# Kernel tuning notes

Hardware: AMD Instinct MI355X
Metric: run time of the kernel (lower is better)

Reference implementation:

```python
import jax, jax.numpy as jnp
import numpy as np

B, N, DIM = 2, 2048, 1024
HEADS, DIM_HEAD = 16, 64
INNER = HEADS * DIM_HEAD  # 1024
SCALE = DIM_HEAD ** -0.5


def setup_inputs() -> dict:
    key = jax.random.key(0)
    ks = jax.random.split(key, 6)
    s = lambda k, shape, fan: jax.random.normal(k, shape, jnp.float32) * (fan ** -0.5)
    return {
        "x": jax.random.normal(ks[0], (B, N, DIM), jnp.float32),
        "similarity": jax.random.normal(ks[1], (B, N), jnp.float32),
        "Wq": s(ks[2], (DIM, INNER), DIM),
        "Wkv": s(ks[3], (DIM, 2 * INNER), DIM),
        "Wo": s(ks[4], (INNER, DIM), INNER),
        "bo": jnp.zeros((DIM,), jnp.float32),
    }


def reference(x, similarity, Wq, Wkv, Wo, bo):
    b, n, _ = x.shape
    h, d = HEADS, DIM_HEAD
    # projections (context = x, self-attention)
    q = (x @ Wq).reshape(b, n, h, d).transpose(0, 2, 1, 3)        # b h n d
    kv = x @ Wkv                                                   # b n 2*inner
    k, v = jnp.split(kv, 2, axis=-1)
    k = k.reshape(b, n, h, d).transpose(0, 2, 1, 3)
    v = v.reshape(b, n, h, d).transpose(0, 2, 1, 3)
    dots = jnp.einsum('bhid,bhjd->bhij', q, k) * SCALE             # b h n n
    # similarity [b,n] -> broadcast as per-query row bias [b,1,n,1]
    dots = dots + similarity[:, None, :, None]
    attn = jax.nn.softmax(dots, axis=-1)
    out = jnp.einsum('bhij,bhjd->bhid', attn, v)                   # b h n d
    out = out.transpose(0, 2, 1, 3).reshape(b, n, h * d)           # b n inner
    return out @ Wo + bo
```

## Files before the change

### kernel.cpp

```cpp
#include <hip/hip_runtime.h>


typedef __attribute__((ext_vector_type(8))) short short8;
typedef __attribute__((ext_vector_type(4))) float float4_;
typedef __attribute__((ext_vector_type(16))) float floatx16;
typedef __attribute__((ext_vector_type(4))) unsigned short ushort4_;
typedef __attribute__((ext_vector_type(4))) unsigned int uint4_;

#define MFMA(a, b, c) __builtin_amdgcn_mfma_f32_16x16x32_bf16((a), (b), (c), 0, 0, 0)
#define MFMA32(a, b, c) __builtin_amdgcn_mfma_f32_32x32x16_bf16((a), (b), (c), 0, 0, 0)

static __device__ __forceinline__ unsigned short f2bf(float f) {
    union { float f; unsigned int u; } v; v.f = f;
    unsigned int r = v.u + 0x7FFFu + ((v.u >> 16) & 1u);
    return (unsigned short)(r >> 16);
}

static __device__ __forceinline__ void gld16(const void* g, void* l) {
    __builtin_amdgcn_global_load_lds(
        (__attribute__((address_space(1))) void*)(g),
        (__attribute__((address_space(3))) void*)(l), 16, 0, 0);
}

__global__ __launch_bounds__(256) void prep(
    const float* __restrict__ X, const float* __restrict__ Wq,
    const float* __restrict__ Wkv, const float* __restrict__ Wo,
    unsigned short* __restrict__ xb, unsigned short* __restrict__ Wt,
    unsigned short* __restrict__ Wot)
{
    const int bid = blockIdx.x, t = threadIdx.x;
    if (bid >= 1024) {
        const int b = bid - 1024;
        const float4_* src = (const float4_*)X;
        ushort4_* dst = (ushort4_*)xb;
        #pragma unroll
        for (int g = 0; g < 8; ++g) {
            const int idx = b * 2048 + g * 256 + t;
            float4_ v = src[idx];
            ushort4_ o;
            o[0] = f2bf(v[0]); o[1] = f2bf(v[1]);
            o[2] = f2bf(v[2]); o[3] = f2bf(v[3]);
            dst[idx] = o;
        }
        return;
    }
    __shared__ float tile[64][65];
    const float* src; unsigned short* dst; int N, kt, nt, drow0;
    if (bid < 256)      { src = Wq;  N = 1024; kt = bid & 15;       nt = bid >> 4;       dst = Wt;  drow0 = nt * 64; }
    else if (bid < 768) { src = Wkv; N = 2048; kt = (bid-256) & 15; nt = (bid-256) >> 4; dst = Wt;  drow0 = 1024 + nt * 64; }
    else                { src = Wo;  N = 1024; kt = (bid-768) & 15; nt = (bid-768) >> 4; dst = Wot; drow0 = nt * 64; }
    const int k0 = kt * 64, n0 = nt * 64;
    const int r0 = t >> 6, c = t & 63;
    #pragma unroll
    for (int i = 0; i < 16; ++i) {
        const int r = i * 4 + r0;
        tile[r][c] = src[(size_t)(k0 + r) * N + n0 + c];
    }
    __syncthreads();
    #pragma unroll
    for (int i = 0; i < 16; ++i) {
        const int rn = i * 4 + r0;
        dst[(size_t)(drow0 + rn) * 1024 + k0 + c] = f2bf(tile[c][rn]);
    }
}

__global__ __launch_bounds__(256) void qkv_gemm2(
    const unsigned short* __restrict__ xb, const unsigned short* __restrict__ Wt,
    unsigned short* __restrict__ q_ws, unsigned short* __restrict__ k_ws,
    unsigned short* __restrict__ vt_ws)
{
    __shared__ unsigned short As[128 * 64];
    __shared__ unsigned short Bs[128 * 64];
    const int t = threadIdx.x, wave = t >> 6, lane = t & 63;
    const int L = lane & 15, quad = lane >> 4;
    const int xcd = blockIdx.x & 7, idx = blockIdx.x >> 3;
    const int mb = (xcd >> 1) * 8 + (idx & 7);
    const int nb = (xcd & 1) * 12 + (idx >> 3);
    const int m0 = mb * 128, n0 = nb * 128;
    const int wr = wave >> 1, wc = wave & 1;

    float4_ z = {0.f, 0.f, 0.f, 0.f};
    float4_ acc[4][4];
    #pragma unroll
    for (int i = 0; i < 4; ++i)
        #pragma unroll
        for (int j = 0; j < 4; ++j) acc[i][j] = z;

    const unsigned short* gA[4]; const unsigned short* gB[4];
    unsigned short* lA[4]; unsigned short* lB[4];
    #pragma unroll
    for (int j = 0; j < 4; ++j) {
        const int cid = wave * 256 + j * 64 + lane;
        const int row = cid >> 3, pc = cid & 7;
        const int lch = pc ^ (row & 7);
        gA[j] = xb + (size_t)(m0 + row) * 1024 + lch * 8;
        gB[j] = Wt + (size_t)(n0 + row) * 1024 + lch * 8;
        lA[j] = As + wave * 2048 + j * 512;
        lB[j] = Bs + wave * 2048 + j * 512;
    }

    for (int kc = 0; kc < 1024; kc += 64) {
        #pragma unroll
        for (int j = 0; j < 4; ++j) {
            gld16(gA[j] + kc, lA[j]);
            gld16(gB[j] + kc, lB[j]);
        }
        __syncthreads();
        #pragma unroll
        for (int ks = 0; ks < 2; ++ks) {
            short8 af[4], bfr[4];
            #pragma unroll
            for (int mt = 0; mt < 4; ++mt) {
                const int rl = wr * 64 + mt * 16 + L;
                af[mt] = *(const short8*)(As + rl * 64 + (((ks * 4 + quad) ^ (L & 7)) << 3));
            }
            #pragma unroll
            for (int nt = 0; nt < 4; ++nt) {
                const int rl = wc * 64 + nt * 16 + L;
                bfr[nt] = *(const short8*)(Bs + rl * 64 + (((ks * 4 + quad) ^ (L & 7)) << 3));
            }
            #pragma unroll
            for (int mt = 0; mt < 4; ++mt)
                #pragma unroll
                for (int nt = 0; nt < 4; ++nt)
                    acc[mt][nt] = MFMA(af[mt], bfr[nt], acc[mt][nt]);
        }
        __syncthreads();
    }

    const int b = m0 >> 11;
    const int type = n0 >> 10;
    #pragma unroll
    for (int mt = 0; mt < 4; ++mt) {
        const int m = (m0 & 2047) + wr * 64 + mt * 16 + quad * 4;
        #pragma unroll
        for (int nt = 0; nt < 4; ++nt) {
            const int cl = (n0 & 1023) + wc * 64 + nt * 16 + L;
            const int h = cl >> 6, d = cl & 63;
            float4_ v = acc[mt][nt];
            if (type == 0) {
                unsigned short* p = q_ws + ((size_t)(b * 16 + h) * 2048 + m) * 64 + d;
                #pragma unroll
                for (int r = 0; r < 4; ++r) p[(size_t)r * 64] = f2bf(v[r] * 0.18033688011f);
            } else if (type == 1) {
                unsigned short* p = k_ws + (size_t)(b * 16 + h) * 131072
                    + (m >> 5) * 2048 + (d >> 3) * 256 + (m & 31) * 8 + (d & 7);
                #pragma unroll
                for (int r = 0; r < 4; ++r) p[r * 8] = f2bf(v[r]);
            } else {
                ushort4_ pk;
                pk[0] = f2bf(v[0]); pk[1] = f2bf(v[1]);
                pk[2] = f2bf(v[2]); pk[3] = f2bf(v[3]);
                *(ushort4_*)(vt_ws + (size_t)(b * 16 + h) * 131072
                    + (m >> 3) * 512 + d * 8 + (m & 7)) = pk;
            }
        }
    }
}

#define LOADT(k0_, k1_, k2_, k3_, v00_, v10_, v01_, v11_, IT) do {            \
    const unsigned short* kp_ = kbase + (IT) * 2048;                          \
    const unsigned short* vp_ = vbase + (IT) * 2048;                          \
    k0_ = *(const short8*)(kp_);        k1_ = *(const short8*)(kp_ + 512);    \
    k2_ = *(const short8*)(kp_ + 1024); k3_ = *(const short8*)(kp_ + 1536);   \
    v00_ = *(const short8*)(vp_);        v10_ = *(const short8*)(vp_ + 1024); \
    v01_ = *(const short8*)(vp_ + 256);  v11_ = *(const short8*)(vp_ + 1280); \
} while (0)

#define COMPT(k0_, k1_, k2_, k3_, v00_, v10_, v01_, v11_) do {                \
    _Pragma("unroll")                                                         \
    for (int qt = 0; qt < 4; ++qt) {                                          \
        floatx16 s;                                                           \
        _Pragma("unroll")                                                     \
        for (int r = 0; r < 16; ++r) s[r] = 0.f;                              \
        s = MFMA32(k0_, qf[qt][0], s);                                        \
        s = MFMA32(k1_, qf[qt][1], s);                                        \
        s = MFMA32(k2_, qf[qt][2], s);                                        \
        s = MFMA32(k3_, qf[qt][3], s);                                        \
        unsigned int pk[8];                                                   \
        _Pragma("unroll")                                                     \
        for (int d = 0; d < 8; ++d) {                                         \
            union { float f; unsigned int u; } a_, b_;                        \
            a_.f = __builtin_amdgcn_exp2f(s[2 * d]);                          \
            b_.f = __builtin_amdgcn_exp2f(s[2 * d + 1]);                      \
            pk[d] = __builtin_amdgcn_perm(b_.u, a_.u, 0x07060302u);           \
        }                                                                     \
        uint4_ w0_, w1_;                                                      \
        w0_[0] = pk[0]; w0_[1] = pk[1]; w0_[2] = pk[2]; w0_[3] = pk[3];       \
        w1_[0] = pk[4]; w1_[1] = pk[5]; w1_[2] = pk[6]; w1_[3] = pk[7];       \
        short8 pa0 = *(short8*)&w0_, pa1 = *(short8*)&w1_;                    \
        lac[qt] = MFMA32(pa0, ONES, lac[qt]);                                 \
        lac[qt] = MFMA32(pa1, ONES, lac[qt]);                                 \
        o[qt][0] = MFMA32(pa0, v00_, o[qt][0]);                               \
        o[qt][0] = MFMA32(pa1, v10_, o[qt][0]);                               \
        o[qt][1] = MFMA32(pa0, v01_, o[qt][1]);                               \
        o[qt][1] = MFMA32(pa1, v11_, o[qt][1]);                               \
    }                                                                         \
} while (0)

__global__ __launch_bounds__(128, 1) void attn_fwd6(
    const unsigned short* __restrict__ q_ws,
    const unsigned short* __restrict__ k_ws,
    const unsigned short* __restrict__ vt_ws,
    unsigned short* __restrict__ o2)
{
    __shared__ float cb[2][6144];
    const int t = threadIdx.x, wave = t >> 6, lane = t & 63;
    const int l32 = lane & 31, hi = lane >> 5;
    const int xcd = blockIdx.x & 7, loc = blockIdx.x >> 3;
    const int bh = xcd * 4 + (loc >> 4);
    const int qb = loc & 15;

    short8 qf[4][4];
    #pragma unroll
    for (int qt = 0; qt < 4; ++qt) {
        const unsigned short* Qp = q_ws
            + ((size_t)(bh * 2048 + qb * 128 + qt * 32 + l32)) * 64 + hi * 8;
        #pragma unroll
        for (int ks = 0; ks < 4; ++ks)
            qf[qt][ks] = *(const short8*)(Qp + ks * 16);
    }

    const int piRow = (l32 & ~12) | ((l32 & 4) << 1) | ((l32 & 8) >> 1);
    const unsigned short* kbase = k_ws + (size_t)bh * 131072
        + wave * 65536 + hi * 256 + piRow * 8;
    const unsigned short* vbase = vt_ws + (size_t)bh * 131072
        + wave * 65536 + hi * 512 + l32 * 8;

    short8 ONES;
    #pragma unroll
    for (int i = 0; i < 8; ++i) ONES[i] = (short)0x3F80;

    floatx16 o[4][2], lac[4];
    #pragma unroll
    for (int qt = 0; qt < 4; ++qt) {
        #pragma unroll
        for (int r = 0; r < 16; ++r) {
            o[qt][0][r] = 0.f; o[qt][1][r] = 0.f; lac[qt][r] = 0.f;
        }
    }

    short8 kA0, kA1, kA2, kA3, vA00, vA10, vA01, vA11;
    short8 kB0, kB1, kB2, kB3, vB00, vB10, vB01, vB11;
    LOADT(kA0, kA1, kA2, kA3, vA00, vA10, vA01, vA11, 0);

    #pragma unroll 1
    for (int it = 0; it < 32; it += 2) {
        LOADT(kB0, kB1, kB2, kB3, vB00, vB10, vB01, vB11, it + 1);
        COMPT(kA0, kA1, kA2, kA3, vA00, vA10, vA01, vA11);
        LOADT(kA0, kA1, kA2, kA3, vA00, vA10, vA01, vA11, (it + 2) & 31);
        COMPT(kB0, kB1, kB2, kB3, vB00, vB10, vB01, vB11);
    }

    float* myb = cb[wave];
    const int don = wave ? 0 : 2;
    #pragma unroll
    for (int g = 0; g < 2; ++g) {
        const int qt = don + g;
        #pragma unroll
        for (int r = 0; r < 16; ++r) {
            myb[(g * 48 + r)      * 64 + lane] = o[qt][0][r];
            myb[(g * 48 + 16 + r) * 64 + lane] = o[qt][1][r];
            myb[(g * 48 + 32 + r) * 64 + lane] = lac[qt][r];
        }
    }
    __syncthreads();
    const float* otb = cb[wave ^ 1];
    const int own = wave ? 2 : 0;
    const int b = bh >> 4, h = bh & 15;
    unsigned short* obase = o2 + ((size_t)(b * 2048 + qb * 128)) * 1024 + h * 64;
    #pragma unroll
    for (int g = 0; g < 2; ++g) {
        const int qt = own + g;
        #pragma unroll
        for (int r = 0; r < 16; ++r) {
            const float o0v = o[qt][0][r] + otb[(g * 48 + r)      * 64 + lane];
            const float o1v = o[qt][1][r] + otb[(g * 48 + 16 + r) * 64 + lane];
            const float lv  = lac[qt][r]  + otb[(g * 48 + 32 + r) * 64 + lane];
            const float iv = 1.0f / lv;
            const int row = qt * 32 + (r & 3) + 8 * (r >> 2) + 4 * hi;
            obase[(size_t)row * 1024 + l32]      = f2bf(o0v * iv);
            obase[(size_t)row * 1024 + 32 + l32] = f2bf(o1v * iv);
        }
    }
}

__global__ __launch_bounds__(256) void out_gemm2(
    const unsigned short* __restrict__ o2, const unsigned short* __restrict__ Wot,
    const float* __restrict__ bo, float* __restrict__ Out)
{
    __shared__ unsigned short As[128 * 64];
    __shared__ unsigned short Bs[64 * 64];
    const int t = threadIdx.x, wave = t >> 6, lane = t & 63;
    const int L = lane & 15, quad = lane >> 4;
    const int xcd = blockIdx.x & 7, idx = blockIdx.x >> 3;
    const int mb = (xcd >> 1) * 8 + (idx & 7);
    const int nb = (xcd & 1) * 8 + (idx >> 3);
    const int m0 = mb * 128, n0 = nb * 64;
    const int wr = wave >> 1, wc = wave & 1;

    float4_ z = {0.f, 0.f, 0.f, 0.f};
    float4_ acc[4][2];
    #pragma unroll
    for (int i = 0; i < 4; ++i)
        #pragma unroll
        for (int j = 0; j < 2; ++j) acc[i][j] = z;

    const unsigned short* gA[4]; unsigned short* lA[4];
    #pragma unroll
    for (int j = 0; j < 4; ++j) {
        const int cid = wave * 256 + j * 64 + lane;
        const int row = cid >> 3, pc = cid & 7;
        gA[j] = o2 + (size_t)(m0 + row) * 1024 + (pc ^ (row & 7)) * 8;
        lA[j] = As + wave * 2048 + j * 512;
    }
    const unsigned short* gB[2]; unsigned short* lB[2];
    #pragma unroll
    for (int j = 0; j < 2; ++j) {
        const int cid = wave * 128 + j * 64 + lane;
        const int row = cid >> 3, pc = cid & 7;
        gB[j] = Wot + (size_t)(n0 + row) * 1024 + (pc ^ (row & 7)) * 8;
        lB[j] = Bs + wave * 1024 + j * 512;
    }

    for (int kc = 0; kc < 1024; kc += 64) {
        #pragma unroll
        for (int j = 0; j < 4; ++j) gld16(gA[j] + kc, lA[j]);
        #pragma unroll
        for (int j = 0; j < 2; ++j) gld16(gB[j] + kc, lB[j]);
        __syncthreads();
        #pragma unroll
        for (int ks = 0; ks < 2; ++ks) {
            short8 af[4], bfr[2];
            #pragma unroll
            for (int mt = 0; mt < 4; ++mt) {
                const int rl = wr * 64 + mt * 16 + L;
                af[mt] = *(const short8*)(As + rl * 64 + (((ks * 4 + quad) ^ (L & 7)) << 3));
            }
            #pragma unroll
            for (int nt = 0; nt < 2; ++nt) {
                const int rl = wc * 32 + nt * 16 + L;
                bfr[nt] = *(const short8*)(Bs + rl * 64 + (((ks * 4 + quad) ^ (L & 7)) << 3));
            }
            #pragma unroll
            for (int mt = 0; mt < 4; ++mt)
                #pragma unroll
                for (int nt = 0; nt < 2; ++nt)
                    acc[mt][nt] = MFMA(af[mt], bfr[nt], acc[mt][nt]);
        }
        __syncthreads();
    }

    #pragma unroll
    for (int mt = 0; mt < 4; ++mt) {
        const int m = m0 + wr * 64 + mt * 16 + quad * 4;
        #pragma unroll
        for (int nt = 0; nt < 2; ++nt) {
            const int c = n0 + wc * 32 + nt * 16 + L;
            const float bias = bo[c];
            #pragma unroll
            for (int r = 0; r < 4; ++r)
                Out[(size_t)(m + r) * 1024 + c] = acc[mt][nt][r] + bias;
        }
    }
}

extern "C" void kernel_launch(void* const* d_in, const int* in_sizes, int n_in,
                              void* d_out, int out_size, void* d_ws, size_t ws_size,
                              hipStream_t stream) {
    const float* x   = (const float*)d_in[0];
    const float* Wq  = (const float*)d_in[2];
    const float* Wkv = (const float*)d_in[3];
    const float* Wo  = (const float*)d_in[4];
    const float* bo  = (const float*)d_in[5];
    float* out = (float*)d_out;

    char* ws = (char*)d_ws;
    const size_t MB = 1024 * 1024;
    unsigned short* xb   = (unsigned short*)(ws);
    unsigned short* o2   = xb;
    unsigned short* Wt   = (unsigned short*)(ws + 8 * MB);
    unsigned short* Wot  = (unsigned short*)(ws + 14 * MB);
    unsigned short* q_ws = (unsigned short*)(ws + 16 * MB);
    unsigned short* k_ws = (unsigned short*)(ws + 24 * MB);
    unsigned short* vt_ws= (unsigned short*)(ws + 32 * MB);

    prep<<<dim3(1536), dim3(256), 0, stream>>>(x, Wq, Wkv, Wo, xb, Wt, Wot);
    qkv_gemm2<<<dim3(768), dim3(256), 0, stream>>>(xb, Wt, q_ws, k_ws, vt_ws);
    attn_fwd6<<<dim3(512), dim3(128), 0, stream>>>(q_ws, k_ws, vt_ws, o2);
    out_gemm2<<<dim3(512), dim3(256), 0, stream>>>(o2, Wot, bo, out);
}
```

Baseline: 203.2 us.

## Halve attention query tile, double grid, and compute softmax row sums on VALU

The attention kernel now handles 64 query rows per block instead of 128, launches 1024 blocks, and declares launch bounds allowing two blocks per CU, which lowers register pressure and raises occupancy. The row-sum accumulation that used extra MFMAs against a ones vector is replaced by scalar VALU adds of the exponentials, combined across lane halves with a shuffle and across waves through shared memory. This removes a third of the matrix ops in the inner loop and shrinks the shared-memory reduction buffer. In exchange, each K/V tile is reused by half as many queries, which doubles K/V load traffic per query.

```diff
diff --git a/kernel.cpp b/kernel.cpp
--- a/kernel.cpp
+++ b/kernel.cpp
@@ -169,7 +169,7 @@
 
 #define COMPT(k0_, k1_, k2_, k3_, v00_, v10_, v01_, v11_) do {                \
     _Pragma("unroll")                                                         \
-    for (int qt = 0; qt < 4; ++qt) {                                          \
+    for (int qt = 0; qt < 2; ++qt) {                                          \
         floatx16 s;                                                           \
         _Pragma("unroll")                                                     \
         for (int r = 0; r < 16; ++r) s[r] = 0.f;                              \
@@ -178,19 +178,20 @@
         s = MFMA32(k2_, qf[qt][2], s);                                        \
         s = MFMA32(k3_, qf[qt][3], s);                                        \
         unsigned int pk[8];                                                   \
+        float ls_ = 0.f;                                                      \
         _Pragma("unroll")                                                     \
         for (int d = 0; d < 8; ++d) {                                         \
             union { float f; unsigned int u; } a_, b_;                        \
             a_.f = __builtin_amdgcn_exp2f(s[2 * d]);                          \
             b_.f = __builtin_amdgcn_exp2f(s[2 * d + 1]);                      \
+            ls_ += a_.f + b_.f;                                               \
             pk[d] = __builtin_amdgcn_perm(b_.u, a_.u, 0x07060302u);           \
         }                                                                     \
+        lsum[qt] += ls_;                                                      \
         uint4_ w0_, w1_;                                                      \
         w0_[0] = pk[0]; w0_[1] = pk[1]; w0_[2] = pk[2]; w0_[3] = pk[3];       \
         w1_[0] = pk[4]; w1_[1] = pk[5]; w1_[2] = pk[6]; w1_[3] = pk[7];       \
         short8 pa0 = *(short8*)&w0_, pa1 = *(short8*)&w1_;                    \
-        lac[qt] = MFMA32(pa0, ONES, lac[qt]);                                 \
-        lac[qt] = MFMA32(pa1, ONES, lac[qt]);                                 \
         o[qt][0] = MFMA32(pa0, v00_, o[qt][0]);                               \
         o[qt][0] = MFMA32(pa1, v10_, o[qt][0]);                               \
         o[qt][1] = MFMA32(pa0, v01_, o[qt][1]);                               \
@@ -198,24 +199,25 @@
     }                                                                         \
 } while (0)
 
-__global__ __launch_bounds__(128, 1) void attn_fwd6(
+__global__ __launch_bounds__(128, 2) void attn_fwd7(
     const unsigned short* __restrict__ q_ws,
     const unsigned short* __restrict__ k_ws,
     const unsigned short* __restrict__ vt_ws,
     unsigned short* __restrict__ o2)
 {
-    __shared__ float cb[2][6144];
+    __shared__ float cbuf[2][2048];
+    __shared__ float lsd[2][2][32];
     const int t = threadIdx.x, wave = t >> 6, lane = t & 63;
     const int l32 = lane & 31, hi = lane >> 5;
     const int xcd = blockIdx.x & 7, loc = blockIdx.x >> 3;
-    const int bh = xcd * 4 + (loc >> 4);
-    const int qb = loc & 15;
-
-    short8 qf[4][4];
-    #pragma unroll
-    for (int qt = 0; qt < 4; ++qt) {
+    const int bh = xcd * 4 + (loc >> 5);
+    const int qb = loc & 31;
+
+    short8 qf[2][4];
+    #pragma unroll
+    for (int qt = 0; qt < 2; ++qt) {
         const unsigned short* Qp = q_ws
-            + ((size_t)(bh * 2048 + qb * 128 + qt * 32 + l32)) * 64 + hi * 8;
+            + ((size_t)(bh * 2048 + qb * 64 + qt * 32 + l32)) * 64 + hi * 8;
         #pragma unroll
         for (int ks = 0; ks < 4; ++ks)
             qf[qt][ks] = *(const short8*)(Qp + ks * 16);
@@ -227,18 +229,12 @@
     const unsigned short* vbase = vt_ws + (size_t)bh * 131072
         + wave * 65536 + hi * 512 + l32 * 8;
 
-    short8 ONES;
-    #pragma unroll
-    for (int i = 0; i < 8; ++i) ONES[i] = (short)0x3F80;
-
-    floatx16 o[4][2], lac[4];
-    #pragma unroll
-    for (int qt = 0; qt < 4; ++qt) {
-        #pragma unroll
-        for (int r = 0; r < 16; ++r) {
-            o[qt][0][r] = 0.f; o[qt][1][r] = 0.f; lac[qt][r] = 0.f;
-        }
-    }
+    floatx16 o[2][2];
+    float lsum[2] = {0.f, 0.f};
+    #pragma unroll
+    for (int qt = 0; qt < 2; ++qt)
+        #pragma unroll
+        for (int r = 0; r < 16; ++r) { o[qt][0][r] = 0.f; o[qt][1][r] = 0.f; }
 
     short8 kA0, kA1, kA2, kA3, vA00, vA10, vA01, vA11;
     short8 kB0, kB1, kB2, kB3, vB00, vB10, vB01, vB11;
@@ -252,36 +248,33 @@
         COMPT(kB0, kB1, kB2, kB3, vB00, vB10, vB01, vB11);
     }
 
-    float* myb = cb[wave];
-    const int don = wave ? 0 : 2;
-    #pragma unroll
-    for (int g = 0; g < 2; ++g) {
-        const int qt = don + g;
-        #pragma unroll
-        for (int r = 0; r < 16; ++r) {
-            myb[(g * 48 + r)      * 64 + lane] = o[qt][0][r];
-            myb[(g * 48 + 16 + r) * 64 + lane] = o[qt][1][r];
-            myb[(g * 48 + 32 + r) * 64 + lane] = lac[qt][r];
-        }
+    #pragma unroll
+    for (int qt = 0; qt < 2; ++qt) {
+        float ltot = lsum[qt] + __shfl_xor(lsum[qt], 32);
+        lsd[wave][qt][l32] = ltot;
+    }
+
+    const int qtd = wave ^ 1;
+    float* myb = cbuf[wave];
+    #pragma unroll
+    for (int r = 0; r < 16; ++r) {
+        myb[r * 64 + lane]        = o[qtd][0][r];
+        myb[(16 + r) * 64 + lane] = o[qtd][1][r];
     }
     __syncthreads();
-    const float* otb = cb[wave ^ 1];
-    const int own = wave ? 2 : 0;
+    const float* otb = cbuf[wave ^ 1];
+    const int qto = wave;
     const int b = bh >> 4, h = bh & 15;
-    unsigned short* obase = o2 + ((size_t)(b * 2048 + qb * 128)) * 1024 + h * 64;
-    #pragma unroll
-    for (int g = 0; g < 2; ++g) {
-        const int qt = own + g;
-        #pragma unroll
-        for (int r = 0; r < 16; ++r) {
-            const float o0v = o[qt][0][r] + otb[(g * 48 + r)      * 64 + lane];
-            const float o1v = o[qt][1][r] + otb[(g * 48 + 16 + r) * 64 + lane];
-            const float lv  = lac[qt][r]  + otb[(g * 48 + 32 + r) * 64 + lane];
-            const float iv = 1.0f / lv;
-            const int row = qt * 32 + (r & 3) + 8 * (r >> 2) + 4 * hi;
-            obase[(size_t)row * 1024 + l32]      = f2bf(o0v * iv);
-            obase[(size_t)row * 1024 + 32 + l32] = f2bf(o1v * iv);
-        }
+    unsigned short* obase = o2 + ((size_t)(b * 2048 + qb * 64)) * 1024 + h * 64;
+    #pragma unroll
+    for (int r = 0; r < 16; ++r) {
+        const int rowloc = (r & 3) + 8 * (r >> 2) + 4 * hi;
+        const float o0v = o[qto][0][r] + otb[r * 64 + lane];
+        const float o1v = o[qto][1][r] + otb[(16 + r) * 64 + lane];
+        const float iv = 1.0f / (lsd[0][qto][rowloc] + lsd[1][qto][rowloc]);
+        const int row = qto * 32 + rowloc;
+        obase[(size_t)row * 1024 + l32]      = f2bf(o0v * iv);
+        obase[(size_t)row * 1024 + 32 + l32] = f2bf(o1v * iv);
     }
 }
 
@@ -387,6 +380,6 @@
 
     prep<<<dim3(1536), dim3(256), 0, stream>>>(x, Wq, Wkv, Wo, xb, Wt, Wot);
     qkv_gemm2<<<dim3(768), dim3(256), 0, stream>>>(xb, Wt, q_ws, k_ws, vt_ws);
-    attn_fwd6<<<dim3(512), dim3(128), 0, stream>>>(q_ws, k_ws, vt_ws, o2);
+    attn_fwd7<<<dim3(1024), dim3(128), 0, stream>>>(q_ws, k_ws, vt_ws, o2);
     out_gemm2<<<dim3(512), dim3(256), 0, stream>>>(o2, Wot, bo, out);
 }
```

Result: faster. 195.3 us (-3.9%).
